# Optimization experiments

Measured on AMD Instinct MI355X. Metric: run time of the kernel, lower is better.

The kernel has to match this reference:

```python
import jax, jax.numpy as jnp
import numpy as np

T = 100000  # context_window
H = 256     # hidden_dim


def setup_inputs() -> dict:
    key = jax.random.key(0)
    k1, k2, k3, k4, k5 = jax.random.split(key, 5)
    inputs = jax.random.normal(k1, (T, H), dtype=jnp.float32)
    hc = jax.random.normal(k2, (1, H), dtype=jnp.float32)
    # learned params (original inits Wm/V to ones; random values give a better numeric test)
    Wm = jax.random.normal(k3, (H, H), dtype=jnp.float32) * (1.0 / np.sqrt(H))
    V = jax.random.normal(k4, (H, 1), dtype=jnp.float32) * (1.0 / np.sqrt(H))
    W1 = jax.random.normal(k5, (H, H), dtype=jnp.float32) * (1.0 / np.sqrt(H))
    return {"inputs": inputs, "hc": hc, "Wm": Wm, "V": V, "W1": W1}


def reference(inputs, hc, Wm, V, W1):
    # Mt: (T, H); broadcast-add the projected context vector to every row
    Mt = inputs
    proj_hc = hc @ W1.T                      # (1, H), torch Linear: x @ W^T
    At = jnp.tanh(Mt @ Wm + proj_hc) @ V     # (T, 1)
    alphat = jax.nn.log_softmax(At.reshape(1, -1), axis=1)  # (1, T)
    ct = alphat @ Mt                         # (1, H) — weighted sum with LOG-softmax weights (faithful)
    return (alphat, ct)
```

## Files before the change

kernel.cpp:

```cpp
#include <hip/hip_runtime.h>
#include <math.h>

#define T_N 100000
#define H_N 256
#define NT16 (T_N / 16)
#define NB_AT 256
#define NWAVES (NB_AT * 12)

typedef __attribute__((ext_vector_type(8))) __bf16 bf16x8;
typedef __attribute__((ext_vector_type(4))) float f32x4;


__device__ __forceinline__ float tanh_fast(float x) {
    float e = __expf(2.0f * x);
    return 1.0f - 2.0f / (e + 1.0f);
}

__global__ __launch_bounds__(256) void k_prep(const float* __restrict__ Wm,
                                              const float* __restrict__ hc,
                                              const float* __restrict__ W1,
                                              __bf16* __restrict__ WmT,
                                              float* __restrict__ proj,
                                              float* __restrict__ s1g,
                                              float* __restrict__ s0g) {
    const int j = blockIdx.x;
    const int t = threadIdx.x;
    WmT[j * H_N + t] = (__bf16)Wm[t * H_N + j];
    __shared__ float red[H_N];
    red[t] = hc[t] * W1[j * H_N + t];
    __syncthreads();
    for (int off = 128; off > 0; off >>= 1) {
        if (t < off) red[t] += red[t + off];
        __syncthreads();
    }
    if (t == 0) proj[j] = red[0];
    if (j == 0) { s1g[t] = 0.0f; s0g[t] = 0.0f; }
}

__global__ __launch_bounds__(768, 2) void k_at(const float* __restrict__ Mt,
                                               const __bf16* __restrict__ WmT,
                                               const float* __restrict__ proj,
                                               const float* __restrict__ V,
                                               float* __restrict__ At,
                                               float2* __restrict__ part2,
                                               float* __restrict__ s1g,
                                               float* __restrict__ s0g) {
    const int tid = threadIdx.x;
    const int lane = tid & 63;
    const int w = tid >> 6;
    const int l15 = lane & 15;
    const int lg = lane >> 4;

    struct SMem {
        __align__(16) char sB[131072];
        float pj[256];
        float vj[256];
        float lsem[12], lses[12];
    };
    __shared__ SMem sm;

    for (int g = tid; g < 8192; g += 768) {
        const int n = g >> 5;
        const int c = g & 31;
        const bf16x8 v = *(const bf16x8*)(WmT + n * H_N + c * 8);
        *(bf16x8*)(&sm.sB[(n * 512 + c * 16) ^ ((n & 7) << 4)]) = v;
    }
    if (tid < 256) { sm.pj[tid] = proj[tid]; sm.vj[tid] = V[tid]; }
    __syncthreads();

    const int gw = blockIdx.x * 12 + w;
    float lm = -1e30f, ls = 0.0f;
    float s1a[4] = {0.f, 0.f, 0.f, 0.f};
    float s0a[4] = {0.f, 0.f, 0.f, 0.f};

    for (int tile = gw; tile < NT16; tile += NWAVES) {
        const float* arow = Mt + (size_t)(tile * 16 + l15) * H_N;

        bf16x8 af[8];
#pragma unroll
        for (int ks = 0; ks < 8; ++ks) {
            const float4 a0 = *(const float4*)(arow + 32 * ks + 8 * lg);
            const float4 a1 = *(const float4*)(arow + 32 * ks + 8 * lg + 4);
            af[ks][0] = (__bf16)a0.x; af[ks][1] = (__bf16)a0.y;
            af[ks][2] = (__bf16)a0.z; af[ks][3] = (__bf16)a0.w;
            af[ks][4] = (__bf16)a1.x; af[ks][5] = (__bf16)a1.y;
            af[ks][6] = (__bf16)a1.z; af[ks][7] = (__bf16)a1.w;
        }

        float pacc[4] = {0.f, 0.f, 0.f, 0.f};
#pragma unroll 2
        for (int jb = 0; jb < 16; ++jb) {
            f32x4 acc = {0.f, 0.f, 0.f, 0.f};
            const int n = 16 * jb + l15;
            const int nb = n * 512;
            const int nswz = (n & 7) << 4;
#pragma unroll
            for (int ks = 0; ks < 8; ++ks) {
                const bf16x8 bf = *(const bf16x8*)(
                    &sm.sB[nb + (((32 * ks + 8 * lg) * 2) ^ nswz)]);
                acc = __builtin_amdgcn_mfma_f32_16x16x32_bf16(af[ks], bf, acc, 0, 0, 0);
            }
            const float pjv = sm.pj[n], vjv = sm.vj[n];
#pragma unroll
            for (int i = 0; i < 4; ++i)
                pacc[i] += tanh_fast(acc[i] + pjv) * vjv;
        }

        float p[4];
#pragma unroll
        for (int i = 0; i < 4; ++i) {
            float q = pacc[i];
            q += __shfl_xor(q, 1);
            q += __shfl_xor(q, 2);
            q += __shfl_xor(q, 4);
            q += __shfl_xor(q, 8);
            p[i] = q;
        }
        if (l15 == 0) {
#pragma unroll
            for (int i = 0; i < 4; ++i) {
                const float at = p[i];
                At[tile * 16 + 4 * lg + i] = at;
                if (at > lm) { ls = ls * __expf(lm - at) + 1.0f; lm = at; }
                else ls += __expf(at - lm);
            }
        }

        const float* crow = Mt + (size_t)tile * 16 * H_N + lane * 4;
        float4 x[16];
#pragma unroll
        for (int r = 0; r < 16; ++r)
            x[r] = *(const float4*)(crow + (size_t)r * H_N);
#pragma unroll
        for (int r = 0; r < 16; ++r) {
            const float atr = __shfl(p[r & 3], 16 * (r >> 2));
            s1a[0] += atr * x[r].x; s1a[1] += atr * x[r].y;
            s1a[2] += atr * x[r].z; s1a[3] += atr * x[r].w;
            s0a[0] += x[r].x; s0a[1] += x[r].y;
            s0a[2] += x[r].z; s0a[3] += x[r].w;
        }
    }

#pragma unroll
    for (int d = 1; d < 64; d <<= 1) {
        const float m2 = __shfl_xor(lm, d), s2 = __shfl_xor(ls, d);
        const float M = fmaxf(lm, m2);
        ls = ls * __expf(lm - M) + s2 * __expf(m2 - M);
        lm = M;
    }
    if (lane == 0) { sm.lsem[w] = lm; sm.lses[w] = ls; }

    __syncthreads();
    float* red1 = (float*)&sm.sB[0];
    float* red2 = (float*)&sm.sB[16384];
#pragma unroll
    for (int q = 0; q < 4; ++q) {
        red1[w * 256 + lane * 4 + q] = s1a[q];
        red2[w * 256 + lane * 4 + q] = s0a[q];
    }
    __syncthreads();
    if (tid < 256) {
        float a = 0.f;
#pragma unroll
        for (int g = 0; g < 12; ++g) a += red1[g * 256 + tid];
        atomicAdd(&s1g[tid], a);
    } else if (tid < 512) {
        const int c = tid - 256;
        float a = 0.f;
#pragma unroll
        for (int g = 0; g < 12; ++g) a += red2[g * 256 + c];
        atomicAdd(&s0g[c], a);
    } else if (tid == 512) {
        float m = sm.lsem[0], s = sm.lses[0];
#pragma unroll
        for (int g = 1; g < 12; ++g) {
            const float m2 = sm.lsem[g], s2 = sm.lses[g];
            const float M = fmaxf(m, m2);
            s = s * __expf(m - M) + s2 * __expf(m2 - M);
            m = M;
        }
        part2[blockIdx.x] = make_float2(m, s);
    }
}

__global__ __launch_bounds__(256) void k_final(const float2* __restrict__ part2,
                                               const float* __restrict__ s1g,
                                               const float* __restrict__ s0g,
                                               float* __restrict__ lse,
                                               float* __restrict__ out) {
    const int tid = threadIdx.x;
    __shared__ float ms[256], ss[256];
    const float2 p = part2[tid];
    ms[tid] = p.x; ss[tid] = p.y;
    __syncthreads();
    for (int off = 128; off > 0; off >>= 1) {
        if (tid < off) {
            const float m2 = ms[tid + off], s2 = ss[tid + off];
            const float M = fmaxf(ms[tid], m2);
            ss[tid] = ss[tid] * __expf(ms[tid] - M) + s2 * __expf(m2 - M);
            ms[tid] = M;
        }
        __syncthreads();
    }
    __shared__ float Ls;
    if (tid == 0) { Ls = ms[0] + logf(ss[0]); *lse = Ls; }
    __syncthreads();
    out[T_N + tid] = s1g[tid] - Ls * s0g[tid];
}

__global__ __launch_bounds__(256) void k_alpha(const float* __restrict__ At,
                                               const float* __restrict__ lse,
                                               float* __restrict__ out) {
    const float L = *lse;
    const int i4 = blockIdx.x * 256 + threadIdx.x;
    if (i4 < T_N / 4) {
        float4 a = *(const float4*)(At + i4 * 4);
        a.x -= L; a.y -= L; a.z -= L; a.w -= L;
        *(float4*)(out + i4 * 4) = a;
    }
}

extern "C" void kernel_launch(void* const* d_in, const int* in_sizes, int n_in,
                              void* d_out, int out_size, void* d_ws, size_t ws_size,
                              hipStream_t stream) {
    const float* inputs = (const float*)d_in[0];
    const float* hc     = (const float*)d_in[1];
    const float* Wm     = (const float*)d_in[2];
    const float* V      = (const float*)d_in[3];
    const float* W1     = (const float*)d_in[4];
    float* out = (float*)d_out;

    char* ws = (char*)d_ws;
    __bf16* WmT  = (__bf16*)ws;
    float* proj  = (float*)(ws + 131072);
    float* At    = (float*)(ws + 132096);
    float2* p2   = (float2*)(ws + 532096);
    float* s1g   = (float*)(ws + 536192);
    float* s0g   = (float*)(ws + 537216);
    float* lse   = (float*)(ws + 538240);

    k_prep<<<256, 256, 0, stream>>>(Wm, hc, W1, WmT, proj, s1g, s0g);
    k_at<<<NB_AT, 768, 0, stream>>>(inputs, WmT, proj, V, At, p2, s1g, s0g);
    k_final<<<1, 256, 0, stream>>>(p2, s1g, s0g, lse, out);
    k_alpha<<<98, 256, 0, stream>>>(At, lse, out);
}
```

Measured before the change: 60.90 us.

## Process two 16-row tiles per wave and share LDS B fragments

Each wave now handles a single 32-row chunk as two 16-row MFMA tiles, so each B fragment read from LDS feeds two MFMAs. The K dimension is also split into two independent accumulator chains to raise instruction-level parallelism. Block size goes to 13 waves, so the 256-block grid covers all 3125 chunks in one pass with no tile loop. In exchange, register pressure roughly doubles for the A fragments, and the stricter launch-bounds occupancy hint may cause spills.

```diff
diff --git a/kernel.cpp b/kernel.cpp
--- a/kernel.cpp
+++ b/kernel.cpp
@@ -3,9 +3,10 @@
 
 #define T_N 100000
 #define H_N 256
-#define NT16 (T_N / 16)
+#define NT32 (T_N / 32)
 #define NB_AT 256
-#define NWAVES (NB_AT * 12)
+#define WPB 13
+#define NTHR (WPB * 64)
 
 typedef __attribute__((ext_vector_type(8))) __bf16 bf16x8;
 typedef __attribute__((ext_vector_type(4))) float f32x4;
@@ -37,14 +38,14 @@
     if (j == 0) { s1g[t] = 0.0f; s0g[t] = 0.0f; }
 }
 
-__global__ __launch_bounds__(768, 2) void k_at(const float* __restrict__ Mt,
-                                               const __bf16* __restrict__ WmT,
-                                               const float* __restrict__ proj,
-                                               const float* __restrict__ V,
-                                               float* __restrict__ At,
-                                               float2* __restrict__ part2,
-                                               float* __restrict__ s1g,
-                                               float* __restrict__ s0g) {
+__global__ __launch_bounds__(NTHR, 4) void k_at(const float* __restrict__ Mt,
+                                                const __bf16* __restrict__ WmT,
+                                                const float* __restrict__ proj,
+                                                const float* __restrict__ V,
+                                                float* __restrict__ At,
+                                                float2* __restrict__ part2,
+                                                float* __restrict__ s1g,
+                                                float* __restrict__ s0g) {
     const int tid = threadIdx.x;
     const int lane = tid & 63;
     const int w = tid >> 6;
@@ -55,11 +56,11 @@
         __align__(16) char sB[131072];
         float pj[256];
         float vj[256];
-        float lsem[12], lses[12];
+        float lsem[WPB], lses[WPB];
     };
     __shared__ SMem sm;
 
-    for (int g = tid; g < 8192; g += 768) {
+    for (int g = tid; g < 8192; g += NTHR) {
         const int n = g >> 5;
         const int c = g & 31;
         const bf16x8 v = *(const bf16x8*)(WmT + n * H_N + c * 8);
@@ -68,76 +69,109 @@
     if (tid < 256) { sm.pj[tid] = proj[tid]; sm.vj[tid] = V[tid]; }
     __syncthreads();
 
-    const int gw = blockIdx.x * 12 + w;
+    const int gw = blockIdx.x * WPB + w;
     float lm = -1e30f, ls = 0.0f;
     float s1a[4] = {0.f, 0.f, 0.f, 0.f};
     float s0a[4] = {0.f, 0.f, 0.f, 0.f};
 
-    for (int tile = gw; tile < NT16; tile += NWAVES) {
-        const float* arow = Mt + (size_t)(tile * 16 + l15) * H_N;
-
-        bf16x8 af[8];
+    if (gw < NT32) {
+        const int t0 = gw * 32;
+        const float* arow0 = Mt + (size_t)(t0 + l15) * H_N;
+        const float* arow1 = Mt + (size_t)(t0 + 16 + l15) * H_N;
+
+        bf16x8 af0[8], af1[8];
 #pragma unroll
         for (int ks = 0; ks < 8; ++ks) {
-            const float4 a0 = *(const float4*)(arow + 32 * ks + 8 * lg);
-            const float4 a1 = *(const float4*)(arow + 32 * ks + 8 * lg + 4);
-            af[ks][0] = (__bf16)a0.x; af[ks][1] = (__bf16)a0.y;
-            af[ks][2] = (__bf16)a0.z; af[ks][3] = (__bf16)a0.w;
-            af[ks][4] = (__bf16)a1.x; af[ks][5] = (__bf16)a1.y;
-            af[ks][6] = (__bf16)a1.z; af[ks][7] = (__bf16)a1.w;
-        }
-
-        float pacc[4] = {0.f, 0.f, 0.f, 0.f};
-#pragma unroll 2
+            const float4 a0 = *(const float4*)(arow0 + 32 * ks + 8 * lg);
+            const float4 a1 = *(const float4*)(arow0 + 32 * ks + 8 * lg + 4);
+            af0[ks][0] = (__bf16)a0.x; af0[ks][1] = (__bf16)a0.y;
+            af0[ks][2] = (__bf16)a0.z; af0[ks][3] = (__bf16)a0.w;
+            af0[ks][4] = (__bf16)a1.x; af0[ks][5] = (__bf16)a1.y;
+            af0[ks][6] = (__bf16)a1.z; af0[ks][7] = (__bf16)a1.w;
+            const float4 b0 = *(const float4*)(arow1 + 32 * ks + 8 * lg);
+            const float4 b1 = *(const float4*)(arow1 + 32 * ks + 8 * lg + 4);
+            af1[ks][0] = (__bf16)b0.x; af1[ks][1] = (__bf16)b0.y;
+            af1[ks][2] = (__bf16)b0.z; af1[ks][3] = (__bf16)b0.w;
+            af1[ks][4] = (__bf16)b1.x; af1[ks][5] = (__bf16)b1.y;
+            af1[ks][6] = (__bf16)b1.z; af1[ks][7] = (__bf16)b1.w;
+        }
+
+        float pacc0[4] = {0.f, 0.f, 0.f, 0.f};
+        float pacc1[4] = {0.f, 0.f, 0.f, 0.f};
+#pragma unroll 1
         for (int jb = 0; jb < 16; ++jb) {
-            f32x4 acc = {0.f, 0.f, 0.f, 0.f};
+            f32x4 a0A = {0.f, 0.f, 0.f, 0.f}, a0B = {0.f, 0.f, 0.f, 0.f};
+            f32x4 a1A = {0.f, 0.f, 0.f, 0.f}, a1B = {0.f, 0.f, 0.f, 0.f};
             const int n = 16 * jb + l15;
             const int nb = n * 512;
             const int nswz = (n & 7) << 4;
 #pragma unroll
-            for (int ks = 0; ks < 8; ++ks) {
-                const bf16x8 bf = *(const bf16x8*)(
+            for (int ks = 0; ks < 4; ++ks) {
+                const bf16x8 bfA = *(const bf16x8*)(
                     &sm.sB[nb + (((32 * ks + 8 * lg) * 2) ^ nswz)]);
-                acc = __builtin_amdgcn_mfma_f32_16x16x32_bf16(af[ks], bf, acc, 0, 0, 0);
+                const bf16x8 bfB = *(const bf16x8*)(
+                    &sm.sB[nb + (((32 * (ks + 4) + 8 * lg) * 2) ^ nswz)]);
+                a0A = __builtin_amdgcn_mfma_f32_16x16x32_bf16(af0[ks], bfA, a0A, 0, 0, 0);
+                a1A = __builtin_amdgcn_mfma_f32_16x16x32_bf16(af1[ks], bfA, a1A, 0, 0, 0);
+                a0B = __builtin_amdgcn_mfma_f32_16x16x32_bf16(af0[ks + 4], bfB, a0B, 0, 0, 0);
+                a1B = __builtin_amdgcn_mfma_f32_16x16x32_bf16(af1[ks + 4], bfB, a1B, 0, 0, 0);
             }
             const float pjv = sm.pj[n], vjv = sm.vj[n];
 #pragma unroll
-            for (int i = 0; i < 4; ++i)
-                pacc[i] += tanh_fast(acc[i] + pjv) * vjv;
-        }
-
-        float p[4];
+            for (int i = 0; i < 4; ++i) {
+                pacc0[i] += tanh_fast(a0A[i] + a0B[i] + pjv) * vjv;
+                pacc1[i] += tanh_fast(a1A[i] + a1B[i] + pjv) * vjv;
+            }
+        }
+
+        float p0[4], p1[4];
 #pragma unroll
         for (int i = 0; i < 4; ++i) {
-            float q = pacc[i];
-            q += __shfl_xor(q, 1);
-            q += __shfl_xor(q, 2);
-            q += __shfl_xor(q, 4);
-            q += __shfl_xor(q, 8);
-            p[i] = q;
+            float q0 = pacc0[i], q1 = pacc1[i];
+            q0 += __shfl_xor(q0, 1); q1 += __shfl_xor(q1, 1);
+            q0 += __shfl_xor(q0, 2); q1 += __shfl_xor(q1, 2);
+            q0 += __shfl_xor(q0, 4); q1 += __shfl_xor(q1, 4);
+            q0 += __shfl_xor(q0, 8); q1 += __shfl_xor(q1, 8);
+            p0[i] = q0; p1[i] = q1;
         }
         if (l15 == 0) {
 #pragma unroll
             for (int i = 0; i < 4; ++i) {
-                const float at = p[i];
-                At[tile * 16 + 4 * lg + i] = at;
-                if (at > lm) { ls = ls * __expf(lm - at) + 1.0f; lm = at; }
-                else ls += __expf(at - lm);
-            }
-        }
-
-        const float* crow = Mt + (size_t)tile * 16 * H_N + lane * 4;
-        float4 x[16];
-#pragma unroll
-        for (int r = 0; r < 16; ++r)
-            x[r] = *(const float4*)(crow + (size_t)r * H_N);
-#pragma unroll
-        for (int r = 0; r < 16; ++r) {
-            const float atr = __shfl(p[r & 3], 16 * (r >> 2));
-            s1a[0] += atr * x[r].x; s1a[1] += atr * x[r].y;
-            s1a[2] += atr * x[r].z; s1a[3] += atr * x[r].w;
-            s0a[0] += x[r].x; s0a[1] += x[r].y;
-            s0a[2] += x[r].z; s0a[3] += x[r].w;
+                const float a0v = p0[i], a1v = p1[i];
+                At[t0 + 4 * lg + i] = a0v;
+                At[t0 + 16 + 4 * lg + i] = a1v;
+                if (a0v > lm) { ls = ls * __expf(lm - a0v) + 1.0f; lm = a0v; }
+                else ls += __expf(a0v - lm);
+                if (a1v > lm) { ls = ls * __expf(lm - a1v) + 1.0f; lm = a1v; }
+                else ls += __expf(a1v - lm);
+            }
+        }
+
+        const float* crow = Mt + (size_t)t0 * H_N + lane * 4;
+        {
+            float4 x[16];
+#pragma unroll
+            for (int r = 0; r < 16; ++r)
+                x[r] = *(const float4*)(crow + (size_t)r * H_N);
+#pragma unroll
+            for (int r = 0; r < 16; ++r) {
+                const float atr = __shfl(p0[r & 3], 16 * (r >> 2));
+                s1a[0] += atr * x[r].x; s1a[1] += atr * x[r].y;
+                s1a[2] += atr * x[r].z; s1a[3] += atr * x[r].w;
+                s0a[0] += x[r].x; s0a[1] += x[r].y;
+                s0a[2] += x[r].z; s0a[3] += x[r].w;
+            }
+#pragma unroll
+            for (int r = 0; r < 16; ++r)
+                x[r] = *(const float4*)(crow + (size_t)(16 + r) * H_N);
+#pragma unroll
+            for (int r = 0; r < 16; ++r) {
+                const float atr = __shfl(p1[r & 3], 16 * (r >> 2));
+                s1a[0] += atr * x[r].x; s1a[1] += atr * x[r].y;
+                s1a[2] += atr * x[r].z; s1a[3] += atr * x[r].w;
+                s0a[0] += x[r].x; s0a[1] += x[r].y;
+                s0a[2] += x[r].z; s0a[3] += x[r].w;
+            }
         }
     }
 
@@ -152,7 +186,7 @@
 
     __syncthreads();
     float* red1 = (float*)&sm.sB[0];
-    float* red2 = (float*)&sm.sB[16384];
+    float* red2 = (float*)&sm.sB[65536];
 #pragma unroll
     for (int q = 0; q < 4; ++q) {
         red1[w * 256 + lane * 4 + q] = s1a[q];
@@ -162,18 +196,18 @@
     if (tid < 256) {
         float a = 0.f;
 #pragma unroll
-        for (int g = 0; g < 12; ++g) a += red1[g * 256 + tid];
+        for (int g = 0; g < WPB; ++g) a += red1[g * 256 + tid];
         atomicAdd(&s1g[tid], a);
     } else if (tid < 512) {
         const int c = tid - 256;
         float a = 0.f;
 #pragma unroll
-        for (int g = 0; g < 12; ++g) a += red2[g * 256 + c];
+        for (int g = 0; g < WPB; ++g) a += red2[g * 256 + c];
         atomicAdd(&s0g[c], a);
     } else if (tid == 512) {
         float m = sm.lsem[0], s = sm.lses[0];
 #pragma unroll
-        for (int g = 1; g < 12; ++g) {
+        for (int g = 1; g < WPB; ++g) {
             const float m2 = sm.lsem[g], s2 = sm.lses[g];
             const float M = fmaxf(m, m2);
             s = s * __expf(m - M) + s2 * __expf(m2 - M);
@@ -240,7 +274,7 @@
     float* lse   = (float*)(ws + 538240);
 
     k_prep<<<256, 256, 0, stream>>>(Wm, hc, W1, WmT, proj, s1g, s0g);
-    k_at<<<NB_AT, 768, 0, stream>>>(inputs, WmT, proj, V, At, p2, s1g, s0g);
+    k_at<<<NB_AT, NTHR, 0, stream>>>(inputs, WmT, proj, V, At, p2, s1g, s0g);
     k_final<<<1, 256, 0, stream>>>(p2, s1g, s0g, lse, out);
     k_alpha<<<98, 256, 0, stream>>>(At, lse, out);
 }
```

Result: faster. 56.56 us (-7.1%).
